# Kernel tuning notes

Measured on AMD Instinct MI355X. Metric: run time of the kernel, lower is better.

## Reference

```python
import jax, jax.numpy as jnp
import numpy as np

B, T, C = 2, 2048, 2048
N_HEAD = 16

def setup_inputs() -> dict:
    key = jax.random.key(0)
    k1, k2, k3 = jax.random.split(key, 3)
    scale = 1.0 / np.sqrt(C)
    return {
        "x": jax.random.normal(k1, (B, T, C), dtype=jnp.float32),
        "w_attn": jax.random.normal(k2, (C, 3 * C), dtype=jnp.float32) * scale,
        "b_attn": jnp.zeros((3 * C,), dtype=jnp.float32),
        "w_proj": jax.random.normal(k3, (C, C), dtype=jnp.float32) * scale,
        "b_proj": jnp.zeros((C,), dtype=jnp.float32),
    }

def reference(x, w_attn, b_attn, w_proj, b_proj):
    Bb, Tt, Cc = x.shape
    hd = Cc // N_HEAD  # head_size
    qkv = x @ w_attn + b_attn              # [B,T,3C]
    q, k, v = jnp.split(qkv, 3, axis=-1)
    # [B,T,C] -> [B,H,T,hd]
    def heads(t):
        return t.reshape(Bb, Tt, N_HEAD, hd).transpose(0, 2, 1, 3)
    q, k, v = heads(q), heads(k), heads(v)
    att = jnp.einsum("bhqd,bhkd->bhqk", q, k) * (hd ** -0.5)
    causal = jnp.tril(jnp.ones((Tt, Tt), dtype=bool))
    att = jnp.where(causal[None, None], att, -jnp.inf)
    att = jax.nn.softmax(att, axis=-1)
    out = jnp.einsum("bhqk,bhkd->bhqd", att, v)
    out = out.transpose(0, 2, 1, 3).reshape(Bb, Tt, Cc)
    return out @ w_proj + b_proj
```

## Files before the change

kernel.cpp:

```cpp
#include <hip/hip_runtime.h>
#include <cstdint>
#include <cstddef>

typedef __bf16 bf16_t;
typedef __bf16 bf16x8 __attribute__((ext_vector_type(8)));
typedef __bf16 bf16x4 __attribute__((ext_vector_type(4)));
typedef float floatx4 __attribute__((ext_vector_type(4)));

#define B_  2
#define T_  2048
#define C_  2048
#define H_  16
#define HD_ 128

#define K_ATTN_SCALE (0.08838834764831843f * 1.44269504088896f)

__device__ __forceinline__ void async_copy16(const void* g, void* l) {
  __builtin_amdgcn_global_load_lds((const __attribute__((address_space(1))) unsigned int*)g,
                                   (__attribute__((address_space(3))) unsigned int*)l,
                                   16, 0, 0);
}

__global__ __launch_bounds__(256) void cvt_f32_bf16(const float* __restrict__ in,
                                                    bf16_t* __restrict__ out, int n4) {
  int i = blockIdx.x * 256 + threadIdx.x;
  if (i >= n4) return;
  const float4 v = ((const float4*)in)[i];
  bf16x4 o;
  o[0] = (bf16_t)v.x; o[1] = (bf16_t)v.y; o[2] = (bf16_t)v.z; o[3] = (bf16_t)v.w;
  ((bf16x4*)out)[i] = o;
}

__global__ __launch_bounds__(256) void transpose_cvt(const float* __restrict__ W,
                                                     bf16_t* __restrict__ Wt,
                                                     int Kd, int Nd) {
  __shared__ float tile[32][33];
  const int tx = threadIdx.x, ty = threadIdx.y;
  const int n0 = blockIdx.x * 32, k0 = blockIdx.y * 32;
#pragma unroll
  for (int j = ty; j < 32; j += 8)
    tile[j][tx] = W[(size_t)(k0 + j) * Nd + n0 + tx];
  __syncthreads();
#pragma unroll
  for (int j = ty; j < 32; j += 8)
    Wt[(size_t)(n0 + j) * Kd + k0 + tx] = (bf16_t)tile[tx][j];
}

__global__ __launch_bounds__(256) void transpose_v(const bf16_t* __restrict__ in,
                                                   bf16_t* __restrict__ out) {
  __shared__ bf16_t tile[32][34];
  const int tx = threadIdx.x, ty = threadIdx.y;
  const int bh = blockIdx.z;
  const int t0 = blockIdx.x * 32, d0 = blockIdx.y * 32;
  const bf16_t* src = in + (size_t)bh * T_ * HD_;
  bf16_t* dst = out + (size_t)bh * T_ * HD_;
#pragma unroll
  for (int j = ty; j < 32; j += 8)
    tile[j][tx] = src[(size_t)(t0 + j) * HD_ + d0 + tx];
  __syncthreads();
#pragma unroll
  for (int j = ty; j < 32; j += 8)
    dst[(size_t)(d0 + j) * T_ + t0 + tx] = tile[tx][j];
}

#define TM 128
#define TN 128
#define BK 64

template <int MODE>
__global__ __launch_bounds__(256) void gemm_bt(
    const bf16_t* __restrict__ A, const bf16_t* __restrict__ Bt,
    const float* __restrict__ bias, float* __restrict__ Cout,
    bf16_t* __restrict__ Qo, bf16_t* __restrict__ Ko, bf16_t* __restrict__ Vo,
    int M, int N, int K) {
  __shared__ bf16_t As[TM][BK];
  __shared__ bf16_t Bs[TN][BK];
  const int tid = threadIdx.x;
  const int wave = tid >> 6, lane = tid & 63;
  const int quad = lane >> 4, l15 = lane & 15;
  const int bm = blockIdx.y * TM, bn = blockIdx.x * TN;
  const int wm = (wave >> 1) * 64, wn = (wave & 1) * 64;
  const int sw = l15 & 7;

  floatx4 acc[4][4] = {};

  for (int k0 = 0; k0 < K; k0 += BK) {
#pragma unroll
    for (int it = 0; it < 4; ++it) {
      int p = it * 4096 + tid * 16;
      int r = p >> 7;
      int cg = ((p >> 4) & 7) ^ (r & 7);
      async_copy16(A + (size_t)(bm + r) * K + k0 + cg * 8, (char*)&As[0][0] + p);
      async_copy16(Bt + (size_t)(bn + r) * K + k0 + cg * 8, (char*)&Bs[0][0] + p);
    }
    __syncthreads();
#pragma unroll
    for (int kc = 0; kc < 2; ++kc) {
      const int cidx = (kc * 4 + quad) ^ sw;
      bf16x8 af[4], bf[4];
#pragma unroll
      for (int i = 0; i < 4; ++i)
        af[i] = *(const bf16x8*)&As[wm + i * 16 + l15][cidx * 8];
#pragma unroll
      for (int j = 0; j < 4; ++j)
        bf[j] = *(const bf16x8*)&Bs[wn + j * 16 + l15][cidx * 8];
#pragma unroll
      for (int i = 0; i < 4; ++i)
#pragma unroll
        for (int j = 0; j < 4; ++j)
          acc[i][j] = __builtin_amdgcn_mfma_f32_16x16x32_bf16(af[i], bf[j], acc[i][j], 0, 0, 0);
    }
    __syncthreads();
  }

#pragma unroll
  for (int i = 0; i < 4; ++i) {
#pragma unroll
    for (int j = 0; j < 4; ++j) {
#pragma unroll
      for (int r = 0; r < 4; ++r) {
        int m = bm + wm + i * 16 + quad * 4 + r;
        int n = bn + wn + j * 16 + l15;
        float val = acc[i][j][r] + bias[n];
        if (MODE == 1) {
          Cout[(size_t)m * N + n] = val;
        } else {
          int which = n >> 11;
          int cc = n & 2047;
          int h = cc >> 7, d = cc & 127;
          int b = m >> 11, t = m & 2047;
          if (which == 0) val *= K_ATTN_SCALE;
          bf16_t bv = (bf16_t)val;
          bf16_t* dst = (which == 0) ? Qo : (which == 1) ? Ko : Vo;
          dst[(((size_t)(b * H_ + h)) * T_ + t) * HD_ + d] = bv;
        }
      }
    }
  }
}

__global__ __launch_bounds__(256) void attn(const bf16_t* __restrict__ Q,
                                            const bf16_t* __restrict__ Kg,
                                            const bf16_t* __restrict__ Vt,
                                            bf16_t* __restrict__ O) {
  __shared__ bf16_t Ks[64][128];
  __shared__ bf16_t Vs[128][64];
  const int tid = threadIdx.x;
  const int wave = tid >> 6, lane = tid & 63;
  const int quad = lane >> 4, l15 = lane & 15;
  const int j = blockIdx.x;
  const int bh = blockIdx.y;
  const int b = bh >> 4, h = bh & 15;
  const int qtA = 31 - j, qtB = j;
  const int nchA = qtA + 1, nchB = qtB + 1;
  const int q0A = qtA * 64 + wave * 16;
  const int q0B = qtB * 64 + wave * 16;

  const bf16_t* Qh = Q + (size_t)bh * T_ * HD_;
  const bf16_t* Kh = Kg + (size_t)bh * T_ * HD_;
  const bf16_t* Vh = Vt + (size_t)bh * HD_ * T_;

  bf16x8 qfA[4], qfB[4];
#pragma unroll
  for (int kk = 0; kk < 4; ++kk) {
    qfA[kk] = *(const bf16x8*)(Qh + (size_t)(q0A + l15) * HD_ + kk * 32 + quad * 8);
    qfB[kk] = *(const bf16x8*)(Qh + (size_t)(q0B + l15) * HD_ + kk * 32 + quad * 8);
  }

  floatx4 oaccA[8] = {}, oaccB[8] = {};
  float l_A = 0.0f, l_B = 0.0f;

  union PU { bf16x4 v; long long u; };
  union PF { long long u[2]; bf16x8 v; };
  const int lo = ((lane & 16) << 1) + l15;

  auto step = [&](const bf16x8* qf, floatx4* oacc, float& l_i, int q0, int kt0, bool mask) {
    floatx4 s[4] = {{}, {}, {}, {}};
#pragma unroll
    for (int st = 0; st < 4; ++st) {
#pragma unroll
      for (int kk = 0; kk < 4; ++kk) {
        bf16x8 kf = *(const bf16x8*)&Ks[st * 16 + l15][(((kk * 4 + quad) ^ l15) & 15) * 8];
        s[st] = __builtin_amdgcn_mfma_f32_16x16x32_bf16(kf, qf[kk], s[st], 0, 0, 0);
      }
    }
    float ps = 0.0f;
    long long pu[4];
#pragma unroll
    for (int st = 0; st < 4; ++st) {
      PU t;
#pragma unroll
      for (int r = 0; r < 4; ++r) {
        float val = s[st][r];
        if (mask) {
          int kt = kt0 + st * 16 + quad * 4 + r;
          val = (kt <= q0 + l15) ? val : -3.0e38f;
        }
        float p = exp2f(val);
        ps += p;
        t.v[r] = (bf16_t)p;
      }
      pu[st] = t.u;
    }
    ps += __shfl_xor(ps, 16);
    ps += __shfl_xor(ps, 32);
    l_i += ps;
#pragma unroll
    for (int bb = 0; bb < 2; ++bb) {
      long long lo0 = __shfl(pu[2 * bb], lo);
      long long hi0 = __shfl(pu[2 * bb], lo + 16);
      long long lo1 = __shfl(pu[2 * bb + 1], lo);
      long long hi1 = __shfl(pu[2 * bb + 1], lo + 16);
      PF pf;
      pf.u[0] = (quad >= 2) ? lo1 : lo0;
      pf.u[1] = (quad >= 2) ? hi1 : hi0;
#pragma unroll
      for (int dt = 0; dt < 8; ++dt) {
        bf16x8 vf = *(const bf16x8*)&Vs[dt * 16 + l15][(((bb * 4 + quad) ^ l15) & 7) * 8];
        oacc[dt] = __builtin_amdgcn_mfma_f32_16x16x32_bf16(pf.v, vf, oacc[dt], 0, 0, 0);
      }
    }
  };

  for (int ch = 0; ch < nchA; ++ch) {
    const int kt0 = ch * 64;
#pragma unroll
    for (int it = 0; it < 4; ++it) {
      int p = it * 4096 + tid * 16;
      int r = p >> 8;
      int cg = ((p >> 4) & 15) ^ (r & 15);
      async_copy16(Kh + (size_t)(kt0 + r) * HD_ + cg * 8, (char*)&Ks[0][0] + p);
    }
#pragma unroll
    for (int it = 0; it < 4; ++it) {
      int p = it * 4096 + tid * 16;
      int r = p >> 7;
      int cg = ((p >> 4) & 7) ^ (r & 7);
      async_copy16(Vh + (size_t)r * T_ + kt0 + cg * 8, (char*)&Vs[0][0] + p);
    }
    __syncthreads();

    step(qfA, oaccA, l_A, q0A, kt0, ch == nchA - 1);
    if (ch < nchB) step(qfB, oaccB, l_B, q0B, kt0, ch == nchB - 1);
    __syncthreads();
  }

  float lrA[4], lrB[4];
#pragma unroll
  for (int r = 0; r < 4; ++r) {
    lrA[r] = __shfl(l_A, quad * 4 + r);
    lrB[r] = __shfl(l_B, quad * 4 + r);
  }
#pragma unroll
  for (int dt = 0; dt < 8; ++dt) {
#pragma unroll
    for (int r = 0; r < 4; ++r) {
      int d = dt * 16 + l15;
      int qa = q0A + quad * 4 + r;
      int qb = q0B + quad * 4 + r;
      O[((size_t)(b * T_ + qa)) * C_ + h * HD_ + d] = (bf16_t)(oaccA[dt][r] / lrA[r]);
      O[((size_t)(b * T_ + qb)) * C_ + h * HD_ + d] = (bf16_t)(oaccB[dt][r] / lrB[r]);
    }
  }
}

extern "C" void kernel_launch(void* const* d_in, const int* in_sizes, int n_in,
                              void* d_out, int out_size, void* d_ws, size_t ws_size,
                              hipStream_t stream) {
  const float* x      = (const float*)d_in[0];
  const float* w_attn = (const float*)d_in[1];
  const float* b_attn = (const float*)d_in[2];
  const float* w_proj = (const float*)d_in[3];
  const float* b_proj = (const float*)d_in[4];
  float* out = (float*)d_out;

  char* p = (char*)d_ws;
  bf16_t* xb  = (bf16_t*)p; p += (size_t)4096 * 2048 * 2;
  bf16_t* waT = (bf16_t*)p; p += (size_t)6144 * 2048 * 2;
  bf16_t* wpT = (bf16_t*)p; p += (size_t)2048 * 2048 * 2;
  bf16_t* Qb  = (bf16_t*)p; p += (size_t)32 * 2048 * 128 * 2;
  bf16_t* Kb  = (bf16_t*)p; p += (size_t)32 * 2048 * 128 * 2;
  bf16_t* Vb  = (bf16_t*)p; p += (size_t)32 * 2048 * 128 * 2;
  bf16_t* Ob  = (bf16_t*)p; p += (size_t)4096 * 2048 * 2;

  cvt_f32_bf16<<<8192, 256, 0, stream>>>(x, xb, 2097152);
  transpose_cvt<<<dim3(6144 / 32, 2048 / 32), dim3(32, 8), 0, stream>>>(w_attn, waT, 2048, 6144);
  transpose_cvt<<<dim3(2048 / 32, 2048 / 32), dim3(32, 8), 0, stream>>>(w_proj, wpT, 2048, 2048);

  gemm_bt<0><<<dim3(6144 / TN, 4096 / TM), 256, 0, stream>>>(
      xb, waT, b_attn, nullptr, Qb, Kb, Ob, 4096, 6144, 2048);

  transpose_v<<<dim3(64, 4, 32), dim3(32, 8), 0, stream>>>(Ob, Vb);

  attn<<<dim3(16, 32), 256, 0, stream>>>(Qb, Kb, Vb, Ob);

  gemm_bt<1><<<dim3(2048 / TN, 4096 / TM), 256, 0, stream>>>(
      Ob, wpT, b_proj, out, nullptr, nullptr, nullptr, 4096, 2048, 2048);
}
```

Baseline: 445.6 us.

## Fuse V transpose into QKV GEMM epilogue and double-buffer attention K/V loads

The QKV GEMM now writes V directly in transposed [bh, d, t] layout. It stages each V tile through swizzled shared memory and stores it with 16-byte vector writes, which removes the separate transpose_v kernel and its extra round trip through global memory. Separately, the attention kernel double-buffers its K/V shared tiles so the next chunk's async loads overlap the current chunk's compute, dropping one barrier per iteration. This doubles attention LDS use to 64KB per block, which may lower occupancy, and the overlap depends on the async LDS loads being ordered correctly by the single barrier.

```diff
diff --git a/kernel.cpp b/kernel.cpp
--- a/kernel.cpp
+++ b/kernel.cpp
@@ -46,23 +46,6 @@
     Wt[(size_t)(n0 + j) * Kd + k0 + tx] = (bf16_t)tile[tx][j];
 }
 
-__global__ __launch_bounds__(256) void transpose_v(const bf16_t* __restrict__ in,
-                                                   bf16_t* __restrict__ out) {
-  __shared__ bf16_t tile[32][34];
-  const int tx = threadIdx.x, ty = threadIdx.y;
-  const int bh = blockIdx.z;
-  const int t0 = blockIdx.x * 32, d0 = blockIdx.y * 32;
-  const bf16_t* src = in + (size_t)bh * T_ * HD_;
-  bf16_t* dst = out + (size_t)bh * T_ * HD_;
-#pragma unroll
-  for (int j = ty; j < 32; j += 8)
-    tile[j][tx] = src[(size_t)(t0 + j) * HD_ + d0 + tx];
-  __syncthreads();
-#pragma unroll
-  for (int j = ty; j < 32; j += 8)
-    dst[(size_t)(d0 + j) * T_ + t0 + tx] = tile[tx][j];
-}
-
 #define TM 128
 #define TN 128
 #define BK 64
@@ -73,8 +56,9 @@
     const float* __restrict__ bias, float* __restrict__ Cout,
     bf16_t* __restrict__ Qo, bf16_t* __restrict__ Ko, bf16_t* __restrict__ Vo,
     int M, int N, int K) {
-  __shared__ bf16_t As[TM][BK];
-  __shared__ bf16_t Bs[TN][BK];
+  __shared__ __align__(16) char smem[32768];
+  bf16_t (*As)[BK] = (bf16_t(*)[BK])smem;
+  bf16_t (*Bs)[BK] = (bf16_t(*)[BK])(smem + 16384);
   const int tid = threadIdx.x;
   const int wave = tid >> 6, lane = tid & 63;
   const int quad = lane >> 4, l15 = lane & 15;
@@ -111,6 +95,36 @@
           acc[i][j] = __builtin_amdgcn_mfma_f32_16x16x32_bf16(af[i], bf[j], acc[i][j], 0, 0, 0);
     }
     __syncthreads();
+  }
+
+  if (MODE == 0 && bn >= 2 * C_) {
+    bf16_t* vt = (bf16_t*)smem;
+    const int h = (bn - 2 * C_) >> 7;
+    const int b = bm >> 11;
+    const int t0g = bm & 2047;
+#pragma unroll
+    for (int i = 0; i < 4; ++i) {
+#pragma unroll
+      for (int j = 0; j < 4; ++j) {
+#pragma unroll
+        for (int r = 0; r < 4; ++r) {
+          int tl = wm + i * 16 + quad * 4 + r;
+          int d  = wn + j * 16 + l15;
+          float val = acc[i][j][r] + bias[bn + wn + j * 16 + l15];
+          vt[d * 128 + (tl ^ (8 * (d & 15)))] = (bf16_t)val;
+        }
+      }
+    }
+    __syncthreads();
+    const int row = tid >> 1, half = tid & 1;
+    bf16_t* dst = Vo + ((size_t)(b * H_ + h) * HD_ + row) * T_ + t0g;
+#pragma unroll
+    for (int cc = 0; cc < 8; ++cc) {
+      int c = half * 8 + cc;
+      uint4 v = *(const uint4*)&vt[row * 128 + ((c ^ (row & 15)) * 8)];
+      *(uint4*)(dst + c * 8) = v;
+    }
+    return;
   }
 
 #pragma unroll
@@ -131,7 +145,7 @@
           int b = m >> 11, t = m & 2047;
           if (which == 0) val *= K_ATTN_SCALE;
           bf16_t bv = (bf16_t)val;
-          bf16_t* dst = (which == 0) ? Qo : (which == 1) ? Ko : Vo;
+          bf16_t* dst = (which == 0) ? Qo : Ko;
           dst[(((size_t)(b * H_ + h)) * T_ + t) * HD_ + d] = bv;
         }
       }
@@ -143,8 +157,8 @@
                                             const bf16_t* __restrict__ Kg,
                                             const bf16_t* __restrict__ Vt,
                                             bf16_t* __restrict__ O) {
-  __shared__ bf16_t Ks[64][128];
-  __shared__ bf16_t Vs[128][64];
+  __shared__ bf16_t Ks[2][64][128];
+  __shared__ bf16_t Vs[2][128][64];
   const int tid = threadIdx.x;
   const int wave = tid >> 6, lane = tid & 63;
   const int quad = lane >> 4, l15 = lane & 15;
@@ -174,13 +188,31 @@
   union PF { long long u[2]; bf16x8 v; };
   const int lo = ((lane & 16) << 1) + l15;
 
-  auto step = [&](const bf16x8* qf, floatx4* oacc, float& l_i, int q0, int kt0, bool mask) {
+  auto stage = [&](int buf, int kt0) {
+#pragma unroll
+    for (int it = 0; it < 4; ++it) {
+      int p = it * 4096 + tid * 16;
+      int r = p >> 8;
+      int cg = ((p >> 4) & 15) ^ (r & 15);
+      async_copy16(Kh + (size_t)(kt0 + r) * HD_ + cg * 8, (char*)&Ks[buf][0][0] + p);
+    }
+#pragma unroll
+    for (int it = 0; it < 4; ++it) {
+      int p = it * 4096 + tid * 16;
+      int r = p >> 7;
+      int cg = ((p >> 4) & 7) ^ (r & 7);
+      async_copy16(Vh + (size_t)r * T_ + kt0 + cg * 8, (char*)&Vs[buf][0][0] + p);
+    }
+  };
+
+  auto step = [&](int buf, const bf16x8* qf, floatx4* oacc, float& l_i, int q0, int kt0,
+                  bool mask) {
     floatx4 s[4] = {{}, {}, {}, {}};
 #pragma unroll
     for (int st = 0; st < 4; ++st) {
 #pragma unroll
       for (int kk = 0; kk < 4; ++kk) {
-        bf16x8 kf = *(const bf16x8*)&Ks[st * 16 + l15][(((kk * 4 + quad) ^ l15) & 15) * 8];
+        bf16x8 kf = *(const bf16x8*)&Ks[buf][st * 16 + l15][(((kk * 4 + quad) ^ l15) & 15) * 8];
         s[st] = __builtin_amdgcn_mfma_f32_16x16x32_bf16(kf, qf[kk], s[st], 0, 0, 0);
       }
     }
@@ -216,33 +248,20 @@
       pf.u[1] = (quad >= 2) ? hi1 : hi0;
 #pragma unroll
       for (int dt = 0; dt < 8; ++dt) {
-        bf16x8 vf = *(const bf16x8*)&Vs[dt * 16 + l15][(((bb * 4 + quad) ^ l15) & 7) * 8];
+        bf16x8 vf = *(const bf16x8*)&Vs[buf][dt * 16 + l15][(((bb * 4 + quad) ^ l15) & 7) * 8];
         oacc[dt] = __builtin_amdgcn_mfma_f32_16x16x32_bf16(pf.v, vf, oacc[dt], 0, 0, 0);
       }
     }
   };
 
+  stage(0, 0);
   for (int ch = 0; ch < nchA; ++ch) {
+    __syncthreads();
+    if (ch + 1 < nchA) stage((ch + 1) & 1, (ch + 1) * 64);
     const int kt0 = ch * 64;
-#pragma unroll
-    for (int it = 0; it < 4; ++it) {
-      int p = it * 4096 + tid * 16;
-      int r = p >> 8;
-      int cg = ((p >> 4) & 15) ^ (r & 15);
-      async_copy16(Kh + (size_t)(kt0 + r) * HD_ + cg * 8, (char*)&Ks[0][0] + p);
-    }
-#pragma unroll
-    for (int it = 0; it < 4; ++it) {
-      int p = it * 4096 + tid * 16;
-      int r = p >> 7;
-      int cg = ((p >> 4) & 7) ^ (r & 7);
-      async_copy16(Vh + (size_t)r * T_ + kt0 + cg * 8, (char*)&Vs[0][0] + p);
-    }
-    __syncthreads();
-
-    step(qfA, oaccA, l_A, q0A, kt0, ch == nchA - 1);
-    if (ch < nchB) step(qfB, oaccB, l_B, q0B, kt0, ch == nchB - 1);
-    __syncthreads();
+    const int buf = ch & 1;
+    step(buf, qfA, oaccA, l_A, q0A, kt0, ch == nchA - 1);
+    if (ch < nchB) step(buf, qfB, oaccB, l_B, q0B, kt0, ch == nchB - 1);
   }
 
   float lrA[4], lrB[4];
@@ -288,9 +307,7 @@
   transpose_cvt<<<dim3(2048 / 32, 2048 / 32), dim3(32, 8), 0, stream>>>(w_proj, wpT, 2048, 2048);
 
   gemm_bt<0><<<dim3(6144 / TN, 4096 / TM), 256, 0, stream>>>(
-      xb, waT, b_attn, nullptr, Qb, Kb, Ob, 4096, 6144, 2048);
-
-  transpose_v<<<dim3(64, 4, 32), dim3(32, 8), 0, stream>>>(Ob, Vb);
+      xb, waT, b_attn, nullptr, Qb, Kb, Vb, 4096, 6144, 2048);
 
   attn<<<dim3(16, 32), 256, 0, stream>>>(Qb, Kb, Vb, Ob);
 
```

Result: faster. 421.0 us (-5.5%).
